# Kernel optimization log

Hardware: AMD Instinct MI355X
Metric: run time of the kernel (lower is better)

Reference implementation:

```python
import jax, jax.numpy as jnp
import numpy as np

T, B, I, H, TAGS = 2048, 64, 50, 100, 6  # H = per-direction LSTM hidden (hidden_dim=100)


def setup_inputs() -> dict:
    key = jax.random.key(0)
    ks = jax.random.split(key, 15)
    s = 0.1
    mk = lambda k, sh: (jax.random.normal(k, sh, dtype=jnp.float32) * s)
    return {
        "x": jax.random.normal(ks[0], (T, B, I), dtype=jnp.float32),
        # forward-direction LSTM (PyTorch gate order i,f,g,o stacked along dim 0)
        "w_ih_f": mk(ks[1], (4 * H, I)), "w_hh_f": mk(ks[2], (4 * H, H)),
        "b_ih_f": mk(ks[3], (4 * H,)), "b_hh_f": mk(ks[4], (4 * H,)),
        # backward-direction LSTM
        "w_ih_b": mk(ks[5], (4 * H, I)), "w_hh_b": mk(ks[6], (4 * H, H)),
        "b_ih_b": mk(ks[7], (4 * H,)), "b_hh_b": mk(ks[8], (4 * H,)),
        # hidden2tag Linear(2H -> TAGS)
        "w_tag": mk(ks[9], (TAGS, 2 * H)), "b_tag": mk(ks[10], (TAGS,)),
        # CRF parameters
        "start_t": mk(ks[11], (TAGS,)), "end_t": mk(ks[12], (TAGS,)),
        "trans": mk(ks[13], (TAGS, TAGS)),
    }


def _lstm_scan(x, w_ih, w_hh, b_ih, b_hh):
    """Single-direction LSTM over leading time axis. x: (T,B,I) -> (T,B,H)."""
    Hh = w_hh.shape[1]
    b = b_ih + b_hh
    xg = jnp.einsum('tbi,gi->tbg', x, w_ih) + b  # precompute input gates (T,B,4H)

    def step(carry, g_in):
        h, c = carry
        g = g_in + h @ w_hh.T
        i, f, gg, o = jnp.split(g, 4, axis=-1)
        c = jax.nn.sigmoid(f) * c + jax.nn.sigmoid(i) * jnp.tanh(gg)
        h = jax.nn.sigmoid(o) * jnp.tanh(c)
        return (h, c), h

    Bn = x.shape[1]
    init = (jnp.zeros((Bn, Hh), x.dtype), jnp.zeros((Bn, Hh), x.dtype))
    _, hs = jax.lax.scan(step, init, xg)
    return hs


def _viterbi(emissions, start_t, end_t, trans):
    """emissions: (T,B,TAGS) -> best tag sequence (T,B) int32."""
    score0 = start_t + emissions[0]  # (B,TAGS)

    def vstep(score, emis_t):
        # score[b,i] + trans[i,j] + emis_t[b,j]
        nxt = score[:, :, None] + trans[None] + emis_t[:, None, :]  # (B,TAGS,TAGS)
        return jnp.max(nxt, axis=1), jnp.argmax(nxt, axis=1).astype(jnp.int32)

    score, bps = jax.lax.scan(vstep, score0, emissions[1:])  # bps: (T-1,B,TAGS)
    last = jnp.argmax(score + end_t, axis=-1).astype(jnp.int32)  # (B,)

    def bstep(tag, bp_t):
        prev = jnp.take_along_axis(bp_t, tag[:, None], axis=1)[:, 0]
        return prev, prev

    _, hist = jax.lax.scan(bstep, last, bps, reverse=True)  # hist[t] = tag at time t, t<T-1
    return jnp.concatenate([hist, last[None]], axis=0)  # (T,B)


def reference(x, w_ih_f, w_hh_f, b_ih_f, b_hh_f, w_ih_b, w_hh_b, b_ih_b, b_hh_b,
              w_tag, b_tag, start_t, end_t, trans):
    h_fwd = _lstm_scan(x, w_ih_f, w_hh_f, b_ih_f, b_hh_f)
    h_bwd = _lstm_scan(x[::-1], w_ih_b, w_hh_b, b_ih_b, b_hh_b)[::-1]
    lstm_out = jnp.concatenate([h_fwd, h_bwd], axis=-1)  # (T,B,2H)
    emissions = jnp.einsum('tbh,gh->tbg', lstm_out, w_tag) + b_tag  # (T,B,TAGS)
    tags = _viterbi(emissions, start_t, end_t, trans)
    return jax.nn.one_hot(tags, TAGS, dtype=jnp.float32)  # (T,B,TAGS)
```

## Files before the change

### kernel.cpp

```cpp
#include <hip/hip_runtime.h>

#define T_LEN 2048
#define BATCH 64
#define IN_DIM 50
#define HID 100
#define NTAGS 6

__device__ __forceinline__ float sigf(float x) { return 1.0f / (1.0f + expf(-x)); }

__device__ __forceinline__ float dpp_xor1(float x) {
    int v = __builtin_amdgcn_update_dpp(0, __float_as_int(x), 0xB1, 0xF, 0xF, true);
    return __int_as_float(v);
}
__device__ __forceinline__ float dpp_xor2(float x) {
    int v = __builtin_amdgcn_update_dpp(0, __float_as_int(x), 0x4E, 0xF, 0xF, true);
    return __int_as_float(v);
}

__global__ __launch_bounds__(512, 1)
void lstm_kernel(const float* __restrict__ x,
                 const float* __restrict__ w_ih_f, const float* __restrict__ w_hh_f,
                 const float* __restrict__ b_ih_f, const float* __restrict__ b_hh_f,
                 const float* __restrict__ w_ih_b, const float* __restrict__ w_hh_b,
                 const float* __restrict__ b_ih_b, const float* __restrict__ b_hh_b,
                 const float* __restrict__ w_tag,
                 float* __restrict__ e_f, float* __restrict__ e_b)
{
    __shared__ __align__(16) float h_ch[2][4][28];
    __shared__ __align__(16) float h_flat[2][HID];
    __shared__ __align__(16) float xb[2][4][16];

    const int tid = threadIdx.x;
    const int b   = blockIdx.x & 63;
    const int dir = blockIdx.x >> 6;

    const float* wih_p = dir ? w_ih_b : w_ih_f;
    const float* whh_p = dir ? w_hh_b : w_hh_f;
    const float* bih_p = dir ? b_ih_b : b_ih_f;
    const float* bhh_p = dir ? b_hh_b : b_hh_f;
    float* e_p = dir ? e_b : e_f;

    {
        float* z1 = &h_ch[0][0][0];
        if (tid < 224) z1[tid] = 0.0f;
        float* z3 = &xb[0][0][0];
        if (tid < 128) z3[tid] = 0.0f;
        float* z2 = &h_flat[0][0];
        if (tid >= 224 && tid < 424) z2[tid - 224] = 0.0f;
    }
    __syncthreads();

    const int u = tid >> 2;
    const int c = tid & 3;
    const int uc = u / 25, uo = u % 25;

    float wx[4][13];
    float wh[4][25];
    float bias4[4];
    if (tid < 400) {
        #pragma unroll
        for (int g = 0; g < 4; ++g) {
            const int row = g * HID + u;
            const float* wri = wih_p + row * IN_DIM;
            #pragma unroll
            for (int m = 0; m < 13; ++m) {
                int i = c * 13 + m;
                wx[g][m] = (i < IN_DIM) ? wri[i] : 0.0f;
            }
            const float* wrh = whh_p + row * HID;
            #pragma unroll
            for (int m = 0; m < 25; ++m) wh[g][m] = wrh[c * 25 + m];
            bias4[g] = bih_p[row] + bhh_p[row];
        }
    }

    const int cw   = tid - 448;
    const int cg   = (cw >= 0) ? (cw >> 3) : 0;
    const int cseg = (cw >= 0) ? (cw & 7) : 0;
    const int u0   = cseg * 13;
    float wt[13];
    if (cw >= 0 && cw < 48) {
        #pragma unroll
        for (int m = 0; m < 13; ++m) {
            int uu = u0 + m;
            wt[m] = (uu < HID) ? w_tag[cg * 200 + dir * HID + uu] : 0.0f;
        }
    }

    const int t0 = dir ? (T_LEN - 1) : 0;
    if (tid < IN_DIM) xb[0][tid / 13][tid % 13] = x[(t0 * BATCH + b) * IN_DIM + tid];
    __syncthreads();

    float c_reg = 0.0f;
    int cur = 0;
    for (int step = 0; step < T_LEN; ++step) {
        const int t = dir ? (T_LEN - 1 - step) : step;
        const int nxt = cur ^ 1;
        if (tid < 400) {
            float4 xq0 = *(const float4*)&xb[cur][c][0];
            float4 xq1 = *(const float4*)&xb[cur][c][4];
            float4 xq2 = *(const float4*)&xb[cur][c][8];
            float x12  = xb[cur][c][12];
            float p0 = 0.f, p1 = 0.f, p2 = 0.f, p3 = 0.f;
            {
                float xv[13] = {xq0.x,xq0.y,xq0.z,xq0.w, xq1.x,xq1.y,xq1.z,xq1.w,
                                xq2.x,xq2.y,xq2.z,xq2.w, x12};
                #pragma unroll
                for (int m = 0; m < 13; ++m) {
                    p0 += xv[m] * wx[0][m];
                    p1 += xv[m] * wx[1][m];
                    p2 += xv[m] * wx[2][m];
                    p3 += xv[m] * wx[3][m];
                }
            }
            #pragma unroll
            for (int mb = 0; mb < 6; ++mb) {
                float4 hq = *(const float4*)&h_ch[cur][c][mb * 4];
                float hv[4] = {hq.x, hq.y, hq.z, hq.w};
                #pragma unroll
                for (int l = 0; l < 4; ++l) {
                    p0 += hv[l] * wh[0][mb * 4 + l];
                    p1 += hv[l] * wh[1][mb * 4 + l];
                    p2 += hv[l] * wh[2][mb * 4 + l];
                    p3 += hv[l] * wh[3][mb * 4 + l];
                }
            }
            {
                float h24 = h_ch[cur][c][24];
                p0 += h24 * wh[0][24];
                p1 += h24 * wh[1][24];
                p2 += h24 * wh[2][24];
                p3 += h24 * wh[3][24];
            }
            p0 += dpp_xor1(p0); p0 += dpp_xor2(p0);
            p1 += dpp_xor1(p1); p1 += dpp_xor2(p1);
            p2 += dpp_xor1(p2); p2 += dpp_xor2(p2);
            p3 += dpp_xor1(p3); p3 += dpp_xor2(p3);
            const float gi = p0 + bias4[0];
            const float gf = p1 + bias4[1];
            const float gg = p2 + bias4[2];
            const float go = p3 + bias4[3];
            c_reg = sigf(gf) * c_reg + sigf(gi) * tanhf(gg);
            const float h = sigf(go) * tanhf(c_reg);
            if (c == 0) {
                h_ch[nxt][uc][uo] = h;
                h_flat[nxt][u]    = h;
            }
        } else if (cw >= 0 && cw < 48) {
            if (step > 0) {
                const int tp = dir ? (t + 1) : (t - 1);
                float p = 0.f;
                #pragma unroll
                for (int m = 0; m < 13; ++m) {
                    int uu = u0 + m;
                    if (uu < HID) p += h_flat[cur][uu] * wt[m];
                }
                p += __shfl_xor(p, 1);
                p += __shfl_xor(p, 2);
                p += __shfl_xor(p, 4);
                if (cseg == 0) e_p[(tp * BATCH + b) * NTAGS + cg] = p;
            }
        } else if (tid >= 496) {
            const int tn = dir ? (t - 1) : (t + 1);
            if (tn >= 0 && tn < T_LEN) {
                const int li = tid - 496;
                #pragma unroll
                for (int m = 0; m < 4; ++m) {
                    int i = li + 16 * m;
                    if (i < IN_DIM) xb[nxt][i / 13][i % 13] = x[(tn * BATCH + b) * IN_DIM + i];
                }
            }
        }
        __syncthreads();
        cur = nxt;
    }
    if (cw >= 0 && cw < 48) {
        const int tp = dir ? 0 : (T_LEN - 1);
        float p = 0.f;
        #pragma unroll
        for (int m = 0; m < 13; ++m) {
            int uu = u0 + m;
            if (uu < HID) p += h_flat[cur][uu] * wt[m];
        }
        p += __shfl_xor(p, 1);
        p += __shfl_xor(p, 2);
        p += __shfl_xor(p, 4);
        if (cseg == 0) e_p[(tp * BATCH + b) * NTAGS + cg] = p;
    }
}

__global__ __launch_bounds__(64, 1)
void viterbi_kernel(const float* __restrict__ e_f, const float* __restrict__ e_b,
                    const float* __restrict__ b_tag, const float* __restrict__ start_t,
                    const float* __restrict__ end_t, const float* __restrict__ trans,
                    float* __restrict__ out)
{
    __shared__ __align__(8) unsigned char bpb[T_LEN][8];
    const int b    = blockIdx.x;
    const int lane = threadIdx.x;
    const int j    = (lane < 6) ? lane : 5;

    float trc[6];
    #pragma unroll
    for (int i = 0; i < 6; ++i) trc[i] = trans[i * 6 + j];
    const float btj = b_tag[j];
    const float stj = start_t[j];
    const float enj = end_t[j];

    float pf[8], pb[8];
    #pragma unroll
    for (int d = 0; d < 8; ++d) {
        const int t = 1 + d;
        pf[d] = e_f[(t * BATCH + b) * NTAGS + j];
        pb[d] = e_b[(t * BATCH + b) * NTAGS + j];
    }
    float scj;
    {
        const float ef0 = e_f[(0 * BATCH + b) * NTAGS + j];
        const float eb0 = e_b[(0 * BATCH + b) * NTAGS + j];
        scj = stj + ((ef0 + eb0) + btj);
    }
    float sc[6];
    #pragma unroll
    for (int i = 0; i < 6; ++i) sc[i] = __shfl(scj, i);

    for (int t = 1; t < T_LEN; ++t) {
        const float ej = (pf[0] + pb[0]) + btj;
        #pragma unroll
        for (int d = 0; d < 7; ++d) { pf[d] = pf[d + 1]; pb[d] = pb[d + 1]; }
        {
            int tl = t + 8; if (tl > T_LEN - 1) tl = T_LEN - 1;
            pf[7] = e_f[(tl * BATCH + b) * NTAGS + j];
            pb[7] = e_b[(tl * BATCH + b) * NTAGS + j];
        }
        float best = (sc[0] + trc[0]) + ej;
        int bi = 0;
        #pragma unroll
        for (int i = 1; i < 6; ++i) {
            float v = (sc[i] + trc[i]) + ej;
            if (v > best) { best = v; bi = i; }
        }
        if (lane < 8) bpb[t][lane] = (unsigned char)bi;
        scj = best;
        #pragma unroll
        for (int i = 0; i < 6; ++i) sc[i] = __shfl(scj, i);
    }

    int tag = 0;
    {
        const float fv = scj + enj;
        float bb = __shfl(fv, 0);
        #pragma unroll
        for (int i = 1; i < 6; ++i) {
            float v = __shfl(fv, i);
            if (v > bb) { bb = v; tag = i; }
        }
    }
    __syncthreads();

    for (int ss = 0; ss < T_LEN / 64; ++ss) {
        const int kbase = (T_LEN - 1) - ss * 64;
        const int myk = kbase - lane;
        unsigned long long row = (myk >= 1) ? *(const unsigned long long*)&bpb[myk][0] : 0ull;
        unsigned rlo = (unsigned)row;
        unsigned rhi = (unsigned)(row >> 32);
        int mytag = 0;
        for (int s = 0; s < 64; ++s) {
            if (s == lane) mytag = tag;
            const int k = kbase - s;
            unsigned lo = __shfl(rlo, s);
            unsigned hi = __shfl(rhi, s);
            if (k >= 1) {
                unsigned vv = (tag < 4) ? lo : hi;
                tag = (int)((vv >> ((tag & 3) * 8)) & 0xFFu);
            }
        }
        const int o = (myk * BATCH + b) * NTAGS;
        #pragma unroll
        for (int jj = 0; jj < 6; ++jj) out[o + jj] = (jj == mytag) ? 1.0f : 0.0f;
    }
}

extern "C" void kernel_launch(void* const* d_in, const int* in_sizes, int n_in,
                              void* d_out, int out_size, void* d_ws, size_t ws_size,
                              hipStream_t stream) {
    const float* x       = (const float*)d_in[0];
    const float* w_ih_f  = (const float*)d_in[1];
    const float* w_hh_f  = (const float*)d_in[2];
    const float* b_ih_f  = (const float*)d_in[3];
    const float* b_hh_f  = (const float*)d_in[4];
    const float* w_ih_b  = (const float*)d_in[5];
    const float* w_hh_b  = (const float*)d_in[6];
    const float* b_ih_b  = (const float*)d_in[7];
    const float* b_hh_b  = (const float*)d_in[8];
    const float* w_tag   = (const float*)d_in[9];
    const float* b_tag   = (const float*)d_in[10];
    const float* start_t = (const float*)d_in[11];
    const float* end_t   = (const float*)d_in[12];
    const float* trans   = (const float*)d_in[13];
    float* out = (float*)d_out;

    float* e_f = (float*)d_ws;
    float* e_b = e_f + (size_t)T_LEN * BATCH * NTAGS;

    lstm_kernel<<<dim3(128), dim3(512), 0, stream>>>(
        x, w_ih_f, w_hh_f, b_ih_f, b_hh_f,
        w_ih_b, w_hh_b, b_ih_b, b_hh_b, w_tag, e_f, e_b);

    viterbi_kernel<<<dim3(64), dim3(64), 0, stream>>>(
        e_f, e_b, b_tag, start_t, end_t, trans, out);
}
```

Baseline: 3.298 ms.

## Restructure Viterbi to one thread per batch with packed backpointers in output

The Viterbi kernel changes from 64 blocks (one wavefront per batch row, one lane per tag with shuffles) to a single block where each thread handles one batch row. That thread keeps all six tag scores in registers and packs the six 3-bit backpointers into a word stored in the output buffer. Backtracking then reads those packed words back in prefetched chunks and overwrites them with one-hot rows, removing per-step cross-lane shuffles and the shared-memory backpointer table. The LSTM kernel's launch attribute also changes to request two waves per EU. The risk is that one workgroup runs on a single CU with serial global-memory round trips per step.

```diff
diff --git a/kernel.cpp b/kernel.cpp
--- a/kernel.cpp
+++ b/kernel.cpp
@@ -17,7 +17,7 @@
     return __int_as_float(v);
 }
 
-__global__ __launch_bounds__(512, 1)
+__global__ __attribute__((amdgpu_flat_work_group_size(512, 512), amdgpu_waves_per_eu(2, 2)))
 void lstm_kernel(const float* __restrict__ x,
                  const float* __restrict__ w_ih_f, const float* __restrict__ w_hh_f,
                  const float* __restrict__ b_ih_f, const float* __restrict__ b_hh_f,
@@ -189,95 +189,141 @@
     }
 }
 
-__global__ __launch_bounds__(64, 1)
-void viterbi_kernel(const float* __restrict__ e_f, const float* __restrict__ e_b,
-                    const float* __restrict__ b_tag, const float* __restrict__ start_t,
-                    const float* __restrict__ end_t, const float* __restrict__ trans,
-                    float* __restrict__ out)
+__global__ void viterbi_scan(const float* __restrict__ e_f, const float* __restrict__ e_b,
+                             const float* __restrict__ b_tag,
+                             const float* __restrict__ start_t, const float* __restrict__ end_t,
+                             const float* __restrict__ trans,
+                             float* __restrict__ out)
 {
-    __shared__ __align__(8) unsigned char bpb[T_LEN][8];
-    const int b    = blockIdx.x;
-    const int lane = threadIdx.x;
-    const int j    = (lane < 6) ? lane : 5;
-
-    float trc[6];
-    #pragma unroll
-    for (int i = 0; i < 6; ++i) trc[i] = trans[i * 6 + j];
-    const float btj = b_tag[j];
-    const float stj = start_t[j];
-    const float enj = end_t[j];
-
-    float pf[8], pb[8];
-    #pragma unroll
-    for (int d = 0; d < 8; ++d) {
-        const int t = 1 + d;
-        pf[d] = e_f[(t * BATCH + b) * NTAGS + j];
-        pb[d] = e_b[(t * BATCH + b) * NTAGS + j];
-    }
-    float scj;
+    const int b = threadIdx.x;
+    const size_t RSTR = (size_t)BATCH * NTAGS;
+
+    float tr[36];
+    #pragma unroll
+    for (int m = 0; m < 36; ++m) tr[m] = trans[m];
+    float bt[6];
+    #pragma unroll
+    for (int j = 0; j < 6; ++j) bt[j] = b_tag[j];
+
+    const float* pf = e_f + (size_t)b * NTAGS;
+    const float* pb = e_b + (size_t)b * NTAGS;
+
+    float sc[6];
+
+    auto loadrow = [&](int t, float2& F0, float2& F1, float2& F2,
+                       float2& B0, float2& B1, float2& B2) {
+        const float* rf = pf + (size_t)t * RSTR;
+        const float* rb = pb + (size_t)t * RSTR;
+        F0 = *(const float2*)(rf);  F1 = *(const float2*)(rf + 2);  F2 = *(const float2*)(rf + 4);
+        B0 = *(const float2*)(rb);  B1 = *(const float2*)(rb + 2);  B2 = *(const float2*)(rb + 4);
+    };
+
+    auto body = [&](int t, float2 F0, float2 F1, float2 F2,
+                    float2 B0, float2 B1, float2 B2) {
+        float ef[6] = {F0.x, F0.y, F1.x, F1.y, F2.x, F2.y};
+        float eb[6] = {B0.x, B0.y, B1.x, B1.y, B2.x, B2.y};
+        unsigned pack = 0;
+        float ns[6];
+        #pragma unroll
+        for (int j = 0; j < 6; ++j) {
+            const float ej = (ef[j] + eb[j]) + bt[j];
+            float v0 = (sc[0] + tr[0 * 6 + j]) + ej;
+            float v1 = (sc[1] + tr[1 * 6 + j]) + ej;
+            float v2 = (sc[2] + tr[2 * 6 + j]) + ej;
+            float v3 = (sc[3] + tr[3 * 6 + j]) + ej;
+            float v4 = (sc[4] + tr[4 * 6 + j]) + ej;
+            float v5 = (sc[5] + tr[5 * 6 + j]) + ej;
+            float best = fmaxf(fmaxf(fmaxf(v0, v1), fmaxf(v2, v3)), fmaxf(v4, v5));
+            int bi = 5;
+            bi = (v4 == best) ? 4 : bi;
+            bi = (v3 == best) ? 3 : bi;
+            bi = (v2 == best) ? 2 : bi;
+            bi = (v1 == best) ? 1 : bi;
+            bi = (v0 == best) ? 0 : bi;
+            ns[j] = best;
+            pack |= (unsigned)bi << (3 * j);
+        }
+        *(unsigned*)(out + ((size_t)(t - 1) * BATCH + b) * NTAGS) = pack;
+        #pragma unroll
+        for (int j = 0; j < 6; ++j) sc[j] = ns[j];
+    };
+
     {
-        const float ef0 = e_f[(0 * BATCH + b) * NTAGS + j];
-        const float eb0 = e_b[(0 * BATCH + b) * NTAGS + j];
-        scj = stj + ((ef0 + eb0) + btj);
-    }
-    float sc[6];
-    #pragma unroll
-    for (int i = 0; i < 6; ++i) sc[i] = __shfl(scj, i);
-
-    for (int t = 1; t < T_LEN; ++t) {
-        const float ej = (pf[0] + pb[0]) + btj;
-        #pragma unroll
-        for (int d = 0; d < 7; ++d) { pf[d] = pf[d + 1]; pb[d] = pb[d + 1]; }
-        {
-            int tl = t + 8; if (tl > T_LEN - 1) tl = T_LEN - 1;
-            pf[7] = e_f[(tl * BATCH + b) * NTAGS + j];
-            pb[7] = e_b[(tl * BATCH + b) * NTAGS + j];
-        }
-        float best = (sc[0] + trc[0]) + ej;
-        int bi = 0;
-        #pragma unroll
-        for (int i = 1; i < 6; ++i) {
-            float v = (sc[i] + trc[i]) + ej;
-            if (v > best) { best = v; bi = i; }
-        }
-        if (lane < 8) bpb[t][lane] = (unsigned char)bi;
-        scj = best;
-        #pragma unroll
-        for (int i = 0; i < 6; ++i) sc[i] = __shfl(scj, i);
-    }
+        float2 F0, F1, F2, B0, B1, B2;
+        loadrow(0, F0, F1, F2, B0, B1, B2);
+        float ef[6] = {F0.x, F0.y, F1.x, F1.y, F2.x, F2.y};
+        float eb[6] = {B0.x, B0.y, B1.x, B1.y, B2.x, B2.y};
+        #pragma unroll
+        for (int j = 0; j < 6; ++j) sc[j] = start_t[j] + ((ef[j] + eb[j]) + bt[j]);
+    }
+
+    float2 fA0, fA1, fA2, bA0, bA1, bA2;
+    float2 fB0, fB1, fB2, bB0, bB1, bB2;
+    loadrow(1, fA0, fA1, fA2, bA0, bA1, bA2);
+    loadrow(2, fB0, fB1, fB2, bB0, bB1, bB2);
+
+    for (int t = 1; t <= T_LEN - 3; t += 2) {
+        body(t, fA0, fA1, fA2, bA0, bA1, bA2);
+        loadrow(t + 2, fA0, fA1, fA2, bA0, bA1, bA2);
+        body(t + 1, fB0, fB1, fB2, bB0, bB1, bB2);
+        { int tl = t + 3; if (tl > T_LEN - 1) tl = T_LEN - 1; loadrow(tl, fB0, fB1, fB2, bB0, bB1, bB2); }
+    }
+    body(T_LEN - 1, fA0, fA1, fA2, bA0, bA1, bA2);
 
     int tag = 0;
     {
-        const float fv = scj + enj;
-        float bb = __shfl(fv, 0);
-        #pragma unroll
-        for (int i = 1; i < 6; ++i) {
-            float v = __shfl(fv, i);
-            if (v > bb) { bb = v; tag = i; }
-        }
-    }
-    __syncthreads();
-
-    for (int ss = 0; ss < T_LEN / 64; ++ss) {
-        const int kbase = (T_LEN - 1) - ss * 64;
-        const int myk = kbase - lane;
-        unsigned long long row = (myk >= 1) ? *(const unsigned long long*)&bpb[myk][0] : 0ull;
-        unsigned rlo = (unsigned)row;
-        unsigned rhi = (unsigned)(row >> 32);
-        int mytag = 0;
-        for (int s = 0; s < 64; ++s) {
-            if (s == lane) mytag = tag;
-            const int k = kbase - s;
-            unsigned lo = __shfl(rlo, s);
-            unsigned hi = __shfl(rhi, s);
-            if (k >= 1) {
-                unsigned vv = (tag < 4) ? lo : hi;
-                tag = (int)((vv >> ((tag & 3) * 8)) & 0xFFu);
-            }
-        }
-        const int o = (myk * BATCH + b) * NTAGS;
-        #pragma unroll
-        for (int jj = 0; jj < 6; ++jj) out[o + jj] = (jj == mytag) ? 1.0f : 0.0f;
+        float best = sc[0] + end_t[0];
+        #pragma unroll
+        for (int j = 1; j < 6; ++j) {
+            float v = sc[j] + end_t[j];
+            if (v > best) { best = v; tag = j; }
+        }
+    }
+
+    __threadfence();
+
+    auto writeoh = [&](int t, int tg) {
+        float* o = out + ((size_t)t * BATCH + b) * NTAGS;
+        o[0] = (tg == 0) ? 1.0f : 0.0f;
+        o[1] = (tg == 1) ? 1.0f : 0.0f;
+        o[2] = (tg == 2) ? 1.0f : 0.0f;
+        o[3] = (tg == 3) ? 1.0f : 0.0f;
+        o[4] = (tg == 4) ? 1.0f : 0.0f;
+        o[5] = (tg == 5) ? 1.0f : 0.0f;
+    };
+    auto stash = [&](int r) -> unsigned {
+        return *(const unsigned*)(out + ((size_t)r * BATCH + b) * NTAGS);
+    };
+
+    writeoh(T_LEN - 1, tag);
+
+    unsigned curw[16], nxtw[16];
+    #pragma unroll
+    for (int s = 0; s < 16; ++s) curw[s] = stash(2046 - s);
+
+    for (int cb = 2046; cb >= 46; cb -= 16) {
+        #pragma unroll
+        for (int s = 0; s < 16; ++s) nxtw[s] = stash(cb - 16 - s);
+        #pragma unroll
+        for (int s = 0; s < 16; ++s) {
+            tag = (int)((curw[s] >> (3 * tag)) & 7u);
+            writeoh(cb - s, tag);
+        }
+        #pragma unroll
+        for (int s = 0; s < 16; ++s) curw[s] = nxtw[s];
+    }
+    #pragma unroll
+    for (int s = 0; s < 16; ++s) {
+        tag = (int)((curw[s] >> (3 * tag)) & 7u);
+        writeoh(30 - s, tag);
+    }
+    unsigned tailw[15];
+    #pragma unroll
+    for (int s = 0; s < 15; ++s) tailw[s] = stash(14 - s);
+    #pragma unroll
+    for (int s = 0; s < 15; ++s) {
+        tag = (int)((tailw[s] >> (3 * tag)) & 7u);
+        writeoh(14 - s, tag);
     }
 }
 
@@ -307,6 +353,6 @@
         x, w_ih_f, w_hh_f, b_ih_f, b_hh_f,
         w_ih_b, w_hh_b, b_ih_b, b_hh_b, w_tag, e_f, e_b);
 
-    viterbi_kernel<<<dim3(64), dim3(64), 0, stream>>>(
+    viterbi_scan<<<dim3(1), dim3(64), 0, stream>>>(
         e_f, e_b, b_tag, start_t, end_t, trans, out);
 }
```

Result: slower. 3.556 ms (+7.8%).
